# Kernel tuning notes

Hardware: AMD Instinct MI355X
Metric: run time of the kernel (lower is better)

Reference implementation:

```python
import jax, jax.numpy as jnp
import numpy as np
from jax import lax

NEG_INF = -1e30

def _binarize(w):
    # BinaryConnect / XNOR-style sign binarization with straight-through estimator
    return w + lax.stop_gradient(jnp.sign(w) - w)

def _conv(x, w, b):
    y = lax.conv_general_dilated(x, w, window_strides=(1, 1), padding='VALID',
                                 dimension_numbers=('NCHW', 'OIHW', 'NCHW'))
    return y + b[None, :, None, None]

def _bn(x, eps, gamma=None, beta=None):
    # training-mode batch norm over (N, H, W)
    mean = jnp.mean(x, axis=(0, 2, 3), keepdims=True)
    var = jnp.var(x, axis=(0, 2, 3), keepdims=True)
    xn = (x - mean) * lax.rsqrt(var + eps)
    if gamma is not None:
        g = jnp.clip(gamma, 0.01, None)  # torch forward clamps BN weight to >=0.01
        xn = xn * g[None, :, None, None] + beta[None, :, None, None]
    return xn

def _maxpool2(x):
    return lax.reduce_window(x, NEG_INF, lax.max, (1, 1, 2, 2), (1, 1, 2, 2), 'VALID')


def setup_inputs() -> dict:
    key = jax.random.key(0)
    ks = jax.random.split(key, 12)
    f = jnp.float32
    return {
        'x': jax.random.normal(ks[0], (8192, 1, 32, 32), dtype=f),
        'conv1_w': jax.random.normal(ks[1], (6, 1, 5, 5), dtype=f) * 0.2,
        'conv1_b': jnp.zeros((6,), dtype=f),
        'conv2_w': jax.random.normal(ks[2], (16, 6, 5, 5), dtype=f) * 0.1,
        'conv2_b': jnp.zeros((16,), dtype=f),
        'bn2_g': jnp.ones((16,), dtype=f),
        'bn2_b': jnp.zeros((16,), dtype=f),
        'conv3_w': jax.random.normal(ks[3], (120, 16, 5, 5), dtype=f) * 0.05,
        'conv3_b': jnp.zeros((120,), dtype=f),
        'bn3_g': jnp.ones((120,), dtype=f),
        'bn3_b': jnp.zeros((120,), dtype=f),
        'fc1_w': jax.random.normal(ks[4], (84, 120), dtype=f) * 0.09,
        'fc1_b': jnp.zeros((84,), dtype=f),
        'fc2_w': jax.random.normal(ks[5], (10, 84), dtype=f) * 0.1,
        'fc2_b': jnp.zeros((10,), dtype=f),
    }


def reference(x, conv1_w, conv1_b, conv2_w, conv2_b, bn2_g, bn2_b,
              conv3_w, conv3_b, bn3_g, bn3_b, fc1_w, fc1_b, fc2_w, fc2_b):
    # layer1: fp conv -> BN(no affine, eps=1e-4) -> relu -> maxpool  [B,6,14,14]
    h = _maxpool2(jax.nn.relu(_bn(_conv(x, conv1_w, conv1_b), 1e-4)))
    # layer2: binary conv -> BN(affine, eps=1e-4) -> relu -> maxpool [B,16,5,5]
    h = _maxpool2(jax.nn.relu(_bn(_conv(h, _binarize(conv2_w), conv2_b), 1e-4, bn2_g, bn2_b)))
    # layer3: binary conv -> BN(affine, eps=1e-5) -> relu            [B,120,1,1]
    h = jax.nn.relu(_bn(_conv(h, _binarize(conv3_w), conv3_b), 1e-5, bn3_g, bn3_b))
    # layer4: binary linear -> relu -> linear                        [B,10]
    h = h.reshape(h.shape[0], -1)  # [B,120]
    h = jax.nn.relu(h @ _binarize(fc1_w).T + fc1_b)
    return h @ fc2_w.T + fc2_b
```

## Files before the change

kernel.cpp:

```cpp
#include <hip/hip_runtime.h>

#define DEVFN __device__ __forceinline__

DEVFN float sgnf(float x) { return (x > 0.f) ? 1.f : ((x < 0.f) ? -1.f : 0.f); }

DEVFN unsigned short f2bf(float x) {
  unsigned int u = __float_as_uint(x);
  unsigned int r = (u + 0x7fffu + ((u >> 16) & 1u)) >> 16;
  return (unsigned short)r;
}

typedef __attribute__((ext_vector_type(8))) short short8;
typedef __attribute__((ext_vector_type(4))) float f32x4;
typedef __attribute__((ext_vector_type(4))) unsigned int u32x4;

#define SUM1 0
#define SQ1  384
#define SUM2 768
#define SQ2  1792
#define SUM3 2816
#define SQ3  10496
#define DBL_BYTES 145408

#define A1 0
#define C1 8
#define A2 16
#define C2 32
#define A3 48
#define C3 168
#define WFR_OFF  3584
#define WFR2_OFF 54784
#define H1_OFF   69632
#define H2_OFF   (H1_OFF + 8192*1176)
#define Y3_OFF   (H2_OFF + 8192*400)

#define RS 17
#define PLANE 238
#define IMGP 1428

__global__ __launch_bounds__(256, 3) void conv1_prep(
    const float* __restrict__ x, const float* __restrict__ w1,
    const float* __restrict__ b1, float* __restrict__ m1,
    double* __restrict__ sums, const float* __restrict__ w2,
    const float* __restrict__ w3, const float* __restrict__ f1,
    unsigned short* __restrict__ wfr3, unsigned short* __restrict__ wfr,
    unsigned short* __restrict__ wfr2) {
  __shared__ float simg[8 * 1088];
  __shared__ float swtp[6 * 40];
  __shared__ float red[6], redq[6];
  int tid = threadIdx.x;
  if (blockIdx.x >= 1024) {
    int i = (blockIdx.x - 1024) * 256 + tid;
    if (i < 7680) {
      int j = i & 7;
      int t = i >> 3;
      int l = t & 63;
      int c = t >> 6;
      int ch = l & 15;
      int kp = c * 32 + ((l >> 4) << 3) + j;
      int k = kp >> 1;
      int b = k >> 3, kx = k & 7;
      int ci = b / 5, ky = b - 5 * ci;
      float v = (kx < 5) ? sgnf(w2[(ch * 6 + ci) * 25 + ky * 5 + kx]) : 0.f;
      wfr3[i] = f2bf(v);
    }
    if (i < 102400) {
      int j = i & 7;
      int t = i >> 3;
      int l = t & 63;
      int cc = (t >> 6) % 25;
      int nt = (t >> 6) / 25;
      int ch = nt * 16 + (l & 15);
      int kp = cc * 32 + ((l >> 4) << 3) + j;
      float v = (ch < 120) ? sgnf(w3[ch * 400 + (kp >> 1)]) : 0.f;
      wfr[i] = f2bf(v);
    }
    if (i < 24576) {
      int j = i & 7;
      int t = i >> 3;
      int l = t & 63;
      int cc = (t >> 6) & 7;
      int nt = t >> 9;
      int col = nt * 16 + (l & 15);
      int kp = cc * 32 + ((l >> 4) << 3) + j;
      int k = kp >> 1;
      float v = (col < 84 && k < 120) ? sgnf(f1[col * 120 + k]) : 0.f;
      wfr2[i] = f2bf(v);
    }
    return;
  }
  int img0 = blockIdx.x * 8;
  {
    const float2* xg = (const float2*)(x + (size_t)img0 * 1024);
    for (int i2 = tid; i2 < 4096; i2 += 256) {
      int img = i2 >> 9;
      int r = (i2 >> 4) & 31;
      int c2 = i2 & 15;
      *(float2*)&simg[img * 1088 + r * 34 + c2 * 2] = xg[i2];
    }
  }
  for (int i = tid; i < 240; i += 256) {
    int ch = i / 40, k = i - ch * 40;
    swtp[i] = (k < 25) ? w1[ch * 25 + k] : 0.f;
  }
  if (tid < 6) { red[tid] = 0.f; redq[tid] = 0.f; }
  __syncthreads();

  for (int idx = tid; idx < 672; idx += 256) {
    int img = idx / 84;
    int r = idx - img * 84;
    int ch = r / 14;
    int py = r - ch * 14;
    float wr[25];
    {
      const float4* wp = (const float4*)&swtp[ch * 40];
#pragma unroll
      for (int t = 0; t < 6; ++t) {
        float4 v = wp[t];
        wr[4 * t] = v.x; wr[4 * t + 1] = v.y; wr[4 * t + 2] = v.z; wr[4 * t + 3] = v.w;
      }
      wr[24] = swtp[ch * 40 + 24];
    }
    float bb = b1[ch];
    float acc0[28], acc1[28];
#pragma unroll
    for (int o = 0; o < 28; ++o) { acc0[o] = bb; acc1[o] = bb; }
#pragma unroll
    for (int d = 0; d < 6; ++d) {
      int row = 2 * py + d;
      float rb[32];
      const float2* rp = (const float2*)&simg[img * 1088 + row * 34];
#pragma unroll
      for (int t = 0; t < 16; ++t) { float2 v = rp[t]; rb[2 * t] = v.x; rb[2 * t + 1] = v.y; }
      if (d < 5) {
#pragma unroll
        for (int kx = 0; kx < 5; ++kx) {
          float w = wr[d * 5 + kx];
#pragma unroll
          for (int o = 0; o < 28; ++o) acc0[o] = fmaf(rb[o + kx], w, acc0[o]);
        }
      }
      if (d >= 1) {
#pragma unroll
        for (int kx = 0; kx < 5; ++kx) {
          float w = wr[(d - 1) * 5 + kx];
#pragma unroll
          for (int o = 0; o < 28; ++o) acc1[o] = fmaf(rb[o + kx], w, acc1[o]);
        }
      }
    }
    float s = 0.f, s2 = 0.f;
#pragma unroll
    for (int o = 0; o < 28; ++o) {
      s += acc0[o] + acc1[o];
      s2 = fmaf(acc0[o], acc0[o], s2);
      s2 = fmaf(acc1[o], acc1[o], s2);
    }
    atomicAdd(&red[ch], s);
    atomicAdd(&redq[ch], s2);
    float* mp = m1 + (size_t)(img0 + img) * 1176 + ch * 196 + py * 14;
#pragma unroll
    for (int j = 0; j < 7; ++j) {
      float2 v;
      v.x = fmaxf(fmaxf(acc0[4 * j], acc0[4 * j + 1]), fmaxf(acc1[4 * j], acc1[4 * j + 1]));
      v.y = fmaxf(fmaxf(acc0[4 * j + 2], acc0[4 * j + 3]), fmaxf(acc1[4 * j + 2], acc1[4 * j + 3]));
      *(float2*)&mp[2 * j] = v;
    }
  }
  __syncthreads();
  if (tid < 6) {
    int slot = blockIdx.x & 63;
    atomicAdd(&sums[SUM1 + tid * 64 + slot], (double)red[tid]);
    atomicAdd(&sums[SQ1 + tid * 64 + slot], (double)redq[tid]);
  }
}

__global__ __launch_bounds__(256) void finalize_bn(
    const double* __restrict__ sum, const double* __restrict__ sq, int nch,
    double invN, double eps, const float* __restrict__ gamma,
    const float* __restrict__ beta, float* __restrict__ a,
    float* __restrict__ c) {
  int t = blockIdx.x * 256 + threadIdx.x;
  int ch = t >> 6, slot = t & 63;
  if (ch >= nch) return;
  double s = sum[ch * 64 + slot];
  double q = sq[ch * 64 + slot];
#pragma unroll
  for (int off = 32; off > 0; off >>= 1) {
    s += __shfl_down(s, off, 64);
    q += __shfl_down(q, off, 64);
  }
  if (slot == 0) {
    double mean = s * invN;
    double var = q * invN - mean * mean;
    float inv = (float)(1.0 / sqrt(var + eps));
    float g = gamma ? fmaxf(gamma[ch], 0.01f) : 1.f;
    float av = g * inv;
    float cv = (beta ? beta[ch] : 0.f) - (float)mean * av;
    a[ch] = av;
    c[ch] = cv;
  }
}

__global__ __launch_bounds__(256, 4) void conv2_mfma(
    const float* __restrict__ m1, const unsigned short* __restrict__ wfr3,
    const float* __restrict__ b2, const float* __restrict__ scales,
    float* __restrict__ m2, double* __restrict__ sums) {
  __shared__ unsigned int Aim[4 * IMGP];
  __shared__ float sa1[6], sc1[6];
  __shared__ float red[16], redq[16];
  int tid = threadIdx.x;
  int img0 = blockIdx.x * 4;
  if (tid < 6) { sa1[tid] = scales[A1 + tid]; sc1[tid] = scales[C1 + tid]; }
  if (tid < 16) { red[tid] = 0.f; redq[tid] = 0.f; }
  for (int i = tid; i < 1008; i += 256) {
    int c3 = i - (i / 3) * 3;
    int t = i / 3;
    int row = t % 14;
    int t2 = t / 14;
    int ci = t2 % 6, img = t2 / 6;
    Aim[img * IMGP + ci * PLANE + row * RS + 14 + c3] = 0u;
  }
  __syncthreads();
  {
    const float2* mg = (const float2*)(m1 + (size_t)img0 * 1176);
    for (int i2 = tid; i2 < 2352; i2 += 256) {
      int img = i2 / 588;
      int e = (i2 - img * 588) * 2;
      int pl = e / 196;
      int rr = e - pl * 196;
      int row = rr / 14, col = rr - row * 14;
      float a = sa1[pl], c = sc1[pl];
      float2 v = mg[i2];
      float v0 = fmaxf(fmaf(a, v.x, c), 0.f);
      float v1 = fmaxf(fmaf(a, v.y, c), 0.f);
      unsigned int h0 = f2bf(v0);
      unsigned int l0 = f2bf(v0 - __uint_as_float(h0 << 16));
      unsigned int h1 = f2bf(v1);
      unsigned int l1 = f2bf(v1 - __uint_as_float(h1 << 16));
      unsigned int* dst = &Aim[img * IMGP + pl * PLANE + row * RS + col];
      dst[0] = h0 | (l0 << 16);
      dst[1] = h1 | (l1 << 16);
    }
  }
  __syncthreads();

  int lane = tid & 63;
  int wv = tid >> 6;
  const short8* bvec = (const short8*)wfr3;
  short8 bf[15];
#pragma unroll
  for (int c = 0; c < 15; ++c) bf[c] = bvec[c * 64 + lane];
  int ch = lane & 15;
  int ag = lane >> 4;
  int agh = ag >> 1, agl = ag & 1;
  float bb = b2[ch];
  float s0 = 0.f, q0 = 0.f;

  for (int t = wv; t < 25; t += 4) {
    int prd = t * 16 + ch;
    int imr = prd / 100;
    int pos = prd - imr * 100;
    int pb = pos >> 2, q = pos & 3;
    int pyr = pb / 5;
    int py = 2 * pyr + (q >> 1);
    int px = 2 * (pb - pyr * 5) + (q & 1);
    const unsigned int* base = &Aim[imr * IMGP + py * RS + px + agl * 4];
    const unsigned int* bR = base + agh * RS;
    const unsigned int* bW = base + agh * 170;
    f32x4 acc = {0.f, 0.f, 0.f, 0.f};
#pragma unroll
    for (int c = 0; c < 15; ++c) {
      const int b0 = 2 * c;
      const int ci0 = b0 / 5, ky0 = b0 % 5;
      const unsigned int* pc =
          ((ky0 == 4) ? bW : bR) + (ci0 * PLANE + ky0 * RS);
      unsigned int a0 = pc[0], a1 = pc[1], a2 = pc[2], a3 = pc[3];
      union { u32x4 u; short8 s; } ua;
      ua.u = (u32x4){a0, a1, a2, a3};
      acc = __builtin_amdgcn_mfma_f32_16x16x32_bf16(ua.s, bf[c], acc, 0, 0, 0);
    }
    int po = t * 4 + ag;
    int imo = po / 25;
    int pbl = po - imo * 25;
    float v0 = acc[0] + bb, v1 = acc[1] + bb;
    float v2 = acc[2] + bb, v3 = acc[3] + bb;
    s0 += (v0 + v1) + (v2 + v3);
    q0 = fmaf(v0, v0, q0); q0 = fmaf(v1, v1, q0);
    q0 = fmaf(v2, v2, q0); q0 = fmaf(v3, v3, q0);
    float mx = fmaxf(fmaxf(v0, v1), fmaxf(v2, v3));
    m2[(size_t)(img0 + imo) * 400 + ch * 25 + pbl] = mx;
  }
  s0 += __shfl_xor(s0, 16, 64); q0 += __shfl_xor(q0, 16, 64);
  s0 += __shfl_xor(s0, 32, 64); q0 += __shfl_xor(q0, 32, 64);
  if (ag == 0) {
    atomicAdd(&red[ch], s0);
    atomicAdd(&redq[ch], q0);
  }
  __syncthreads();
  if (tid < 16) {
    int slot = blockIdx.x & 63;
    atomicAdd(&sums[SUM2 + tid * 64 + slot], (double)red[tid]);
    atomicAdd(&sums[SQ2 + tid * 64 + slot], (double)redq[tid]);
  }
}

__global__ __launch_bounds__(256) void conv3_mfma(
    const float* __restrict__ m2, const unsigned short* __restrict__ wfr,
    const float* __restrict__ b3, const float* __restrict__ scales,
    float* __restrict__ y3, double* __restrict__ sums) {
  __shared__ unsigned int Alds[16 * 404];
  __shared__ float sa2[16], sc2[16];
  __shared__ float red[128], redq[128];
  int tid = threadIdx.x;
  int img0 = blockIdx.x * 16;
  if (tid < 16) { sa2[tid] = scales[A2 + tid]; sc2[tid] = scales[C2 + tid]; }
  if (tid < 128) { red[tid] = 0.f; redq[tid] = 0.f; }
  __syncthreads();
  for (int i4 = tid; i4 < 1600; i4 += 256) {
    int img = i4 / 100, k4 = i4 - img * 100;
    int k = 4 * k4;
    float4 v = *(const float4*)(m2 + (size_t)(img0 + img) * 400 + k);
    float vv[4] = {v.x, v.y, v.z, v.w};
    unsigned int pk[4];
#pragma unroll
    for (int e = 0; e < 4; ++e) {
      int ch = ((k + e) * 41) >> 10;
      float val = fmaxf(fmaf(sa2[ch], vv[e], sc2[ch]), 0.f);
      unsigned int hb = f2bf(val);
      float vh = __uint_as_float(hb << 16);
      unsigned int lb = f2bf(val - vh);
      pk[e] = hb | (lb << 16);
    }
    unsigned int* dst = &Alds[img * 404 + k];
    dst[0] = pk[0]; dst[1] = pk[1]; dst[2] = pk[2]; dst[3] = pk[3];
  }
  __syncthreads();

  int lane = tid & 63;
  int wv = tid >> 6;
  int nt0 = wv * 2, nt1 = wv * 2 + 1;
  const short8* bvec = (const short8*)wfr;
  int arow = lane & 15;
  int ag = lane >> 4;
  f32x4 acc0 = {0.f, 0.f, 0.f, 0.f}, acc1 = {0.f, 0.f, 0.f, 0.f};
  const unsigned short* abase =
      (const unsigned short*)&Alds[arow * 404 + ag * 4];
#pragma unroll 5
  for (int c = 0; c < 25; ++c) {
    short8 af = *(const short8*)(abase + c * 32);
    short8 b0 = bvec[(nt0 * 25 + c) * 64 + lane];
    short8 b1 = bvec[(nt1 * 25 + c) * 64 + lane];
    acc0 = __builtin_amdgcn_mfma_f32_16x16x32_bf16(af, b0, acc0, 0, 0, 0);
    acc1 = __builtin_amdgcn_mfma_f32_16x16x32_bf16(af, b1, acc1, 0, 0, 0);
  }
  int chA = nt0 * 16 + (lane & 15);
  int chB = nt1 * 16 + (lane & 15);
  int rbase = img0 + ((lane >> 4) << 2);
  {
    float bias = b3[chA];
    float s = 0.f, q = 0.f;
#pragma unroll
    for (int r = 0; r < 4; ++r) {
      float v = acc0[r] + bias;
      y3[(size_t)(rbase + r) * 120 + chA] = v;
      s += v; q = fmaf(v, v, q);
    }
    atomicAdd(&red[chA], s);
    atomicAdd(&redq[chA], q);
  }
  if (chB < 120) {
    float bias = b3[chB];
    float s = 0.f, q = 0.f;
#pragma unroll
    for (int r = 0; r < 4; ++r) {
      float v = acc1[r] + bias;
      y3[(size_t)(rbase + r) * 120 + chB] = v;
      s += v; q = fmaf(v, v, q);
    }
    atomicAdd(&red[chB], s);
    atomicAdd(&redq[chB], q);
  }
  __syncthreads();
  if (tid < 120) {
    int slot = blockIdx.x & 63;
    atomicAdd(&sums[SUM3 + tid * 64 + slot], (double)red[tid]);
    atomicAdd(&sums[SQ3 + tid * 64 + slot], (double)redq[tid]);
  }
}

__global__ __launch_bounds__(192) void fc_mfma(
    const float* __restrict__ y3, const float* __restrict__ scales,
    const unsigned short* __restrict__ wfr2, const float* __restrict__ b1,
    const float* __restrict__ w2, const float* __restrict__ b2,
    float* __restrict__ out) {
  __shared__ unsigned int Alds[16 * 132];
  __shared__ float sh4[16 * 88];
  __shared__ float sw2[10 * 85];
  __shared__ float sa3[120], sc3[120];
  __shared__ float sb1[84], sb2[10];
  int tid = threadIdx.x;
  int img0 = blockIdx.x * 16;
  if (tid < 120) { sa3[tid] = scales[A3 + tid]; sc3[tid] = scales[C3 + tid]; }
  if (tid < 84) sb1[tid] = b1[tid];
  if (tid >= 84 && tid < 94) sb2[tid - 84] = b2[tid - 84];
  for (int i = tid; i < 850; i += 192) {
    int o = i / 85, k = i - o * 85;
    sw2[i] = (k < 84) ? w2[o * 84 + k] : 0.f;
  }
  __syncthreads();
  for (int i4 = tid; i4 < 512; i4 += 192) {
    int img = i4 >> 5, k4 = i4 & 31;
    int k = 4 * k4;
    unsigned int pk[4] = {0u, 0u, 0u, 0u};
    if (k4 < 30) {
      float4 v = *(const float4*)(y3 + (size_t)(img0 + img) * 120 + k);
      float vv[4] = {v.x, v.y, v.z, v.w};
#pragma unroll
      for (int e = 0; e < 4; ++e) {
        float val = fmaxf(fmaf(sa3[k + e], vv[e], sc3[k + e]), 0.f);
        unsigned int hb = f2bf(val);
        float vh = __uint_as_float(hb << 16);
        unsigned int lb = f2bf(val - vh);
        pk[e] = hb | (lb << 16);
      }
    }
    unsigned int* dst = &Alds[img * 132 + k];
    dst[0] = pk[0]; dst[1] = pk[1]; dst[2] = pk[2]; dst[3] = pk[3];
  }
  __syncthreads();

  int lane = tid & 63;
  int wv = tid >> 6;
  int nt0 = wv * 2, nt1 = wv * 2 + 1;
  const short8* bvec = (const short8*)wfr2;
  int arow = lane & 15;
  int ag = lane >> 4;
  f32x4 acc0 = {0.f, 0.f, 0.f, 0.f}, acc1 = {0.f, 0.f, 0.f, 0.f};
  const unsigned short* abase =
      (const unsigned short*)&Alds[arow * 132 + ag * 4];
#pragma unroll
  for (int c = 0; c < 8; ++c) {
    short8 af = *(const short8*)(abase + c * 32);
    short8 b0 = bvec[(nt0 * 8 + c) * 64 + lane];
    short8 b1 = bvec[(nt1 * 8 + c) * 64 + lane];
    acc0 = __builtin_amdgcn_mfma_f32_16x16x32_bf16(af, b0, acc0, 0, 0, 0);
    acc1 = __builtin_amdgcn_mfma_f32_16x16x32_bf16(af, b1, acc1, 0, 0, 0);
  }
  {
    int jA = nt0 * 16 + (lane & 15);
    int jB = nt1 * 16 + (lane & 15);
    int r0 = (lane >> 4) << 2;
#pragma unroll
    for (int r = 0; r < 4; ++r)
      sh4[(r0 + r) * 88 + jA] = fmaxf(acc0[r] + sb1[jA], 0.f);
    if (jB < 84) {
#pragma unroll
      for (int r = 0; r < 4; ++r)
        sh4[(r0 + r) * 88 + jB] = fmaxf(acc1[r] + sb1[jB], 0.f);
    }
  }
  __syncthreads();
  if (tid < 160) {
    int img = tid / 10, o = tid - (tid / 10) * 10;
    float acc = sb2[o];
    const float* hp = &sh4[img * 88];
    const float* wp = &sw2[o * 85];
#pragma unroll 4
    for (int k = 0; k < 84; ++k) acc = fmaf(hp[k], wp[k], acc);
    out[(size_t)(img0 + img) * 10 + o] = acc;
  }
}

extern "C" void kernel_launch(void* const* d_in, const int* in_sizes, int n_in,
                              void* d_out, int out_size, void* d_ws,
                              size_t ws_size, hipStream_t stream) {
  const float* x = (const float*)d_in[0];
  const float* conv1_w = (const float*)d_in[1];
  const float* conv1_b = (const float*)d_in[2];
  const float* conv2_w = (const float*)d_in[3];
  const float* conv2_b = (const float*)d_in[4];
  const float* bn2_g = (const float*)d_in[5];
  const float* bn2_b = (const float*)d_in[6];
  const float* conv3_w = (const float*)d_in[7];
  const float* conv3_b = (const float*)d_in[8];
  const float* bn3_g = (const float*)d_in[9];
  const float* bn3_b = (const float*)d_in[10];
  const float* fc1_w = (const float*)d_in[11];
  const float* fc1_b = (const float*)d_in[12];
  const float* fc2_w = (const float*)d_in[13];
  const float* fc2_b = (const float*)d_in[14];
  float* out = (float*)d_out;

  double* sums = (double*)d_ws;
  float* fbase = (float*)((char*)d_ws + DBL_BYTES);
  float* scales = fbase;
  unsigned short* wfr = (unsigned short*)(fbase + WFR_OFF);
  unsigned short* wfr2 = (unsigned short*)(fbase + WFR2_OFF);
  float* m1 = fbase + H1_OFF;
  float* m2 = fbase + H2_OFF;
  float* y3 = fbase + Y3_OFF;
  unsigned short* wfr3 = (unsigned short*)y3;

  hipMemsetAsync(d_ws, 0, DBL_BYTES, stream);

  conv1_prep<<<1424, 256, 0, stream>>>(x, conv1_w, conv1_b, m1, sums, conv2_w,
                                       conv3_w, fc1_w, wfr3, wfr, wfr2);
  finalize_bn<<<2, 256, 0, stream>>>(sums + SUM1, sums + SQ1, 6,
                                     1.0 / (8192.0 * 784.0), 1e-4, nullptr,
                                     nullptr, scales + A1, scales + C1);

  conv2_mfma<<<2048, 256, 0, stream>>>(m1, wfr3, conv2_b, scales, m2, sums);
  finalize_bn<<<4, 256, 0, stream>>>(sums + SUM2, sums + SQ2, 16,
                                     1.0 / (8192.0 * 100.0), 1e-4, bn2_g, bn2_b,
                                     scales + A2, scales + C2);

  conv3_mfma<<<512, 256, 0, stream>>>(m2, wfr, conv3_b, scales, y3, sums);
  finalize_bn<<<30, 256, 0, stream>>>(sums + SUM3, sums + SQ3, 120,
                                      1.0 / 8192.0, 1e-5, bn3_g, bn3_b,
                                      scales + A3, scales + C3);

  fc_mfma<<<512, 192, 0, stream>>>(y3, scales, wfr2, fc1_b, fc2_w, fc2_b, out);
}
```

Baseline: 194.7 us.

## Interleave image pairs in LDS and use packed FMA for conv1

Stores two images interleaved as float2 pairs in shared memory so each thread computes the same output positions for two images with packed 2-wide FMAs (v_pk_fma_f32). Work is split into half-rows to keep the register count down, and the occupancy hint is raised from 3 to 4 blocks. The aim is to halve FMA instruction count in the conv1 stage. In exchange, max-pool output stores become scalar and strided across two images, and the LDS writes during staging are scattered.

```diff
diff --git a/kernel.cpp b/kernel.cpp
--- a/kernel.cpp
+++ b/kernel.cpp
@@ -12,6 +12,7 @@
 
 typedef __attribute__((ext_vector_type(8))) short short8;
 typedef __attribute__((ext_vector_type(4))) float f32x4;
+typedef __attribute__((ext_vector_type(2))) float f32x2;
 typedef __attribute__((ext_vector_type(4))) unsigned int u32x4;
 
 #define SUM1 0
@@ -38,14 +39,14 @@
 #define PLANE 238
 #define IMGP 1428
 
-__global__ __launch_bounds__(256, 3) void conv1_prep(
+__global__ __launch_bounds__(256, 4) void conv1_prep(
     const float* __restrict__ x, const float* __restrict__ w1,
     const float* __restrict__ b1, float* __restrict__ m1,
     double* __restrict__ sums, const float* __restrict__ w2,
     const float* __restrict__ w3, const float* __restrict__ f1,
     unsigned short* __restrict__ wfr3, unsigned short* __restrict__ wfr,
     unsigned short* __restrict__ wfr2) {
-  __shared__ float simg[8 * 1088];
+  __shared__ f32x2 simg[4 * 1088];
   __shared__ float swtp[6 * 40];
   __shared__ float red[6], redq[6];
   int tid = threadIdx.x;
@@ -94,77 +95,94 @@
     const float2* xg = (const float2*)(x + (size_t)img0 * 1024);
     for (int i2 = tid; i2 < 4096; i2 += 256) {
       int img = i2 >> 9;
-      int r = (i2 >> 4) & 31;
-      int c2 = i2 & 15;
-      *(float2*)&simg[img * 1088 + r * 34 + c2 * 2] = xg[i2];
+      int j = i2 & 511;
+      float2 v = xg[img * 512 + j];
+      int p = img >> 1, q = img & 1;
+      int row = j >> 4, col = (j & 15) * 2;
+      float* d0 = (float*)&simg[p * 1088 + row * 34 + col];
+      d0[q] = v.x;
+      d0[2 + q] = v.y;
     }
   }
   for (int i = tid; i < 240; i += 256) {
-    int ch = i / 40, k = i - ch * 40;
-    swtp[i] = (k < 25) ? w1[ch * 25 + k] : 0.f;
+    int ch = i / 40, r = i - ch * 40;
+    int ky = r >> 3, kx = r & 7;
+    swtp[i] = (kx < 5) ? w1[ch * 25 + ky * 5 + kx] : 0.f;
   }
   if (tid < 6) { red[tid] = 0.f; redq[tid] = 0.f; }
   __syncthreads();
 
   for (int idx = tid; idx < 672; idx += 256) {
-    int img = idx / 84;
-    int r = idx - img * 84;
-    int ch = r / 14;
-    int py = r - ch * 14;
-    float wr[25];
-    {
-      const float4* wp = (const float4*)&swtp[ch * 40];
-#pragma unroll
-      for (int t = 0; t < 6; ++t) {
-        float4 v = wp[t];
-        wr[4 * t] = v.x; wr[4 * t + 1] = v.y; wr[4 * t + 2] = v.z; wr[4 * t + 3] = v.w;
-      }
-      wr[24] = swtp[ch * 40 + 24];
-    }
+    int ch = idx % 6;
+    int t = idx / 6;
+    int h = t & 1;
+    int t2 = t >> 1;
+    int py = t2 % 14;
+    int p = t2 / 14;
     float bb = b1[ch];
-    float acc0[28], acc1[28];
-#pragma unroll
-    for (int o = 0; o < 28; ++o) { acc0[o] = bb; acc1[o] = bb; }
+    f32x2 acc0[14], acc1[14];
+#pragma unroll
+    for (int o = 0; o < 14; ++o) {
+      acc0[o] = (f32x2){bb, bb};
+      acc1[o] = (f32x2){bb, bb};
+    }
+    const f32x2* ibase = &simg[p * 1088 + h * 14];
+    const float* wch = &swtp[ch * 40];
 #pragma unroll
     for (int d = 0; d < 6; ++d) {
       int row = 2 * py + d;
-      float rb[32];
-      const float2* rp = (const float2*)&simg[img * 1088 + row * 34];
-#pragma unroll
-      for (int t = 0; t < 16; ++t) { float2 v = rp[t]; rb[2 * t] = v.x; rb[2 * t + 1] = v.y; }
+      f32x2 rb[18];
+      const f32x4* rp = (const f32x4*)(ibase + row * 34);
+#pragma unroll
+      for (int tt = 0; tt < 9; ++tt) {
+        f32x4 v = rp[tt];
+        rb[2 * tt] = (f32x2){v.x, v.y};
+        rb[2 * tt + 1] = (f32x2){v.z, v.w};
+      }
       if (d < 5) {
+        const float* wrow = wch + d * 8;
+        f32x4 w4 = *(const f32x4*)wrow;
+        float w5[5] = {w4.x, w4.y, w4.z, w4.w, wrow[4]};
 #pragma unroll
         for (int kx = 0; kx < 5; ++kx) {
-          float w = wr[d * 5 + kx];
-#pragma unroll
-          for (int o = 0; o < 28; ++o) acc0[o] = fmaf(rb[o + kx], w, acc0[o]);
+          f32x2 ws = {w5[kx], w5[kx]};
+#pragma unroll
+          for (int o = 0; o < 14; ++o)
+            acc0[o] = __builtin_elementwise_fma(rb[o + kx], ws, acc0[o]);
         }
       }
       if (d >= 1) {
+        const float* wrow = wch + (d - 1) * 8;
+        f32x4 w4 = *(const f32x4*)wrow;
+        float w5[5] = {w4.x, w4.y, w4.z, w4.w, wrow[4]};
 #pragma unroll
         for (int kx = 0; kx < 5; ++kx) {
-          float w = wr[(d - 1) * 5 + kx];
-#pragma unroll
-          for (int o = 0; o < 28; ++o) acc1[o] = fmaf(rb[o + kx], w, acc1[o]);
+          f32x2 ws = {w5[kx], w5[kx]};
+#pragma unroll
+          for (int o = 0; o < 14; ++o)
+            acc1[o] = __builtin_elementwise_fma(rb[o + kx], ws, acc1[o]);
         }
       }
     }
-    float s = 0.f, s2 = 0.f;
-#pragma unroll
-    for (int o = 0; o < 28; ++o) {
-      s += acc0[o] + acc1[o];
-      s2 = fmaf(acc0[o], acc0[o], s2);
-      s2 = fmaf(acc1[o], acc1[o], s2);
-    }
-    atomicAdd(&red[ch], s);
-    atomicAdd(&redq[ch], s2);
-    float* mp = m1 + (size_t)(img0 + img) * 1176 + ch * 196 + py * 14;
+    f32x2 sv = {0.f, 0.f}, qv = {0.f, 0.f};
+#pragma unroll
+    for (int o = 0; o < 14; ++o) {
+      f32x2 a0 = acc0[o], a1 = acc1[o];
+      sv += a0; sv += a1;
+      qv = __builtin_elementwise_fma(a0, a0, qv);
+      qv = __builtin_elementwise_fma(a1, a1, qv);
+    }
+    atomicAdd(&red[ch], sv.x + sv.y);
+    atomicAdd(&redq[ch], qv.x + qv.y);
+    float* mpA = m1 + (size_t)(img0 + 2 * p) * 1176 + ch * 196 + py * 14 + h * 7;
+    float* mpB = mpA + 1176;
 #pragma unroll
     for (int j = 0; j < 7; ++j) {
-      float2 v;
-      v.x = fmaxf(fmaxf(acc0[4 * j], acc0[4 * j + 1]), fmaxf(acc1[4 * j], acc1[4 * j + 1]));
-      v.y = fmaxf(fmaxf(acc0[4 * j + 2], acc0[4 * j + 3]), fmaxf(acc1[4 * j + 2], acc1[4 * j + 3]));
-      *(float2*)&mp[2 * j] = v;
+      f32x2 m = __builtin_elementwise_max(
+          __builtin_elementwise_max(acc0[2 * j], acc0[2 * j + 1]),
+          __builtin_elementwise_max(acc1[2 * j], acc1[2 * j + 1]));
+      mpA[j] = m.x;
+      mpB[j] = m.y;
     }
   }
   __syncthreads();
```

Measured after the change: 190.3 us (median of 2 runs). -2.3%, faster.
